# Performance work log

Measured on AMD Instinct MI355X. Metric: run time of the kernel, lower is better.

## Reference

```python
import jax, jax.numpy as jnp
import numpy as np
from jax import lax

S, B, V, D, H, L, C = 2048, 32, 50000, 512, 512, 2, 10


def setup_inputs() -> dict:
    key = jax.random.key(0)
    ks = jax.random.split(key, 6)
    x = jax.random.randint(ks[0], (S, B), 0, V)  # (seq, batch) token ids
    embed = jax.random.normal(ks[1], (V, D), jnp.float32) * 0.1
    # per layer: W maps input -> [x_tilde, f_gate, r_gate], each H wide
    W = jax.random.normal(ks[2], (L, D, 3 * H), jnp.float32) * (1.0 / np.sqrt(D))
    b = jnp.zeros((L, 2 * H), jnp.float32)  # biases for f and r gates
    Wc = jax.random.normal(ks[3], (H, C), jnp.float32) * 0.05
    bc = jnp.zeros((C,), jnp.float32)
    return {"x": x, "embed": embed, "W": W, "b": b, "Wc": Wc, "bc": bc}


def _sru_layer(h_in, W_l, b_l):
    # h_in: (S, B, H) (input dim == hidden dim -> identity highway skip)
    U = jnp.einsum('sbd,dk->sbk', h_in, W_l)  # (S, B, 3H)
    xt, fg, rg = jnp.split(U, 3, axis=-1)
    bf, br = jnp.split(b_l, 2)
    f = jax.nn.sigmoid(fg + bf)
    r = jax.nn.sigmoid(rg + br)

    def step(c, inp):
        f_t, xt_t = inp
        c = f_t * c + (1.0 - f_t) * xt_t  # elementwise light recurrence
        return c, c

    c0 = jnp.zeros((h_in.shape[1], f.shape[-1]), h_in.dtype)
    _, cs = lax.scan(step, c0, (f, xt))  # cs: (S, B, H)
    # highway output
    return r * jnp.tanh(cs) + (1.0 - r) * h_in


def reference(x, embed, W, b, Wc, bc):
    h = embed[x]  # (S, B, D); dropout layers are identity at inference
    for l in range(W.shape[0]):
        h = _sru_layer(h, W[l], b[l])
    out = jnp.tanh(h)            # (S, B, H)
    pooled = jnp.max(out, axis=0)  # max-pool over time -> (B, H)
    pooled = jnp.tanh(pooled)
    return pooled @ Wc + bc      # (B, C)
```

## Files before the change

### kernel.cpp

```cpp
#include <hip/hip_runtime.h>
#include <cmath>

#define S_LEN 2048
#define B_SZ 32
#define D_DIM 512
#define H_DIM 512
#define C_NUM 10
#define M_ROWS (S_LEN * B_SZ)
#define BH (B_SZ * H_DIM)
#define N_COLS (3 * H_DIM)

#define SC 1024
#define SCH 8
#define NSUB 128
#define CROWS (SC * B_SZ)

typedef __bf16 bf16_t;
typedef bf16_t bf16x8 __attribute__((ext_vector_type(8)));
typedef float f32x4 __attribute__((ext_vector_type(4)));
typedef unsigned short ushort_t;

__device__ __forceinline__ unsigned int f2bf(float f) {
  union { float f; unsigned int u; } a;
  a.f = f;
  unsigned int r = a.u + 0x7FFFu + ((a.u >> 16) & 1u);
  return r >> 16;
}
__device__ __forceinline__ unsigned int pack2bf(float lo, float hi) {
  return f2bf(lo) | (f2bf(hi) << 16);
}
__device__ __forceinline__ float bflo(unsigned int u) {
  union { unsigned int u; float f; } a; a.u = u << 16; return a.f;
}
__device__ __forceinline__ float bfhi(unsigned int u) {
  union { unsigned int u; float f; } a; a.u = u & 0xffff0000u; return a.f;
}
__device__ __forceinline__ float sigf(float x) {
  return 1.f / (1.f + __expf(-x));
}
__device__ __forceinline__ float tanh_fast(float c) {
  float e = __expf(2.f * c);
  return 1.f - 2.f / (e + 1.f);
}
__device__ __forceinline__ void load16_lds(const void* g, void* l) {
  __builtin_amdgcn_global_load_lds(
      (const __attribute__((address_space(1))) unsigned int*)g,
      (__attribute__((address_space(3))) unsigned int*)l, 16, 0, 0);
}


__global__ __launch_bounds__(256) void gather_kernel(const int* __restrict__ x,
                                                     const float* __restrict__ embed,
                                                     uint4* __restrict__ E4) {
  int i = blockIdx.x * blockDim.x + threadIdx.x;
  const int total = M_ROWS * 16;
  int stride = gridDim.x * blockDim.x;
  for (; i < total; i += stride) {
    int m = i >> 4;
    int kg = (i & 15) * 4;
    int tile = m >> 7, row = m & 127;
    int xm = x[m];
    const float4* src = (const float4*)(embed + (size_t)xm * 512 + kg * 8);
    float4 v[8];
#pragma unroll
    for (int j = 0; j < 8; j++) v[j] = src[j];
    uint4* dst = E4 + (size_t)tile * 8192 + row;
#pragma unroll
    for (int j = 0; j < 4; j++) {
      dst[(size_t)(kg + j) * 128] =
          make_uint4(pack2bf(v[2 * j].x, v[2 * j].y), pack2bf(v[2 * j].z, v[2 * j].w),
                     pack2bf(v[2 * j + 1].x, v[2 * j + 1].y),
                     pack2bf(v[2 * j + 1].z, v[2 * j + 1].w));
    }
  }
}

__global__ __launch_bounds__(256) void wt_kernel(const float* __restrict__ W,
                                                 ushort_t* __restrict__ Wt) {
  int e = blockIdx.x * blockDim.x + threadIdx.x;
  if (e >= 2 * 786432) return;
  int l = e / 786432;
  int t = e - l * 786432;
  int ntile = t >> 16;
  int rr = t & 65535;
  int kc = rr >> 10;
  int row = (rr >> 3) & 127;
  int kk = t & 7;
  int n = ntile * 128 + row;
  int k = kc * 8 + kk;
  Wt[e] = (ushort_t)f2bf(W[(size_t)l * D_DIM * N_COLS + (size_t)k * N_COLS + n]);
}

__global__ __launch_bounds__(256, 3) void sru_gemm_bf16(
    const ushort_t* __restrict__ At,
    int tile0,
    const ushort_t* __restrict__ Bt,
    ushort_t* __restrict__ xt_out, ushort_t* __restrict__ f_out,
    ushort_t* __restrict__ r_out) {
  __shared__ ushort_t As[3][4096];
  __shared__ ushort_t Bs[3][4096];
  const int t = threadIdx.x;
  const int wave = t >> 6, lane = t & 63;
  const int cpx = gridDim.x >> 3;
  const int swz = (blockIdx.x & 7) * cpx + (blockIdx.x >> 3);
  const int nb = swz % 12, mb = swz / 12;
  const int m0 = mb * 128, n0 = nb * 128;
  const int wm = wave & 1, wn = wave >> 1;
  const int lrow = lane >> 4, lcol = lane & 15;

  f32x4 acc[4][4];
#pragma unroll
  for (int i = 0; i < 4; i++)
#pragma unroll
    for (int j = 0; j < 4; j++) acc[i][j] = (f32x4){0.f, 0.f, 0.f, 0.f};

  const ushort_t* Ab = At + ((size_t)(tile0 + mb) << 16);
  const ushort_t* Bb = Bt + ((size_t)nb << 16);
  const int c0 = wave * 2;
  const int le = lane * 8;

#define STAGE(buf, k0)                                                      \
  do {                                                                      \
    load16_lds(Ab + (k0) * 128 + (c0 + 0) * 512 + le, &As[buf][(c0 + 0) * 512]); \
    load16_lds(Ab + (k0) * 128 + (c0 + 1) * 512 + le, &As[buf][(c0 + 1) * 512]); \
    load16_lds(Bb + (k0) * 128 + (c0 + 0) * 512 + le, &Bs[buf][(c0 + 0) * 512]); \
    load16_lds(Bb + (k0) * 128 + (c0 + 1) * 512 + le, &Bs[buf][(c0 + 1) * 512]); \
  } while (0)

  STAGE(0, 0);
  STAGE(1, 32);
#pragma unroll
  for (int step = 0; step < 16; ++step) {
    if (step < 15)
      asm volatile("s_waitcnt vmcnt(4)" ::: "memory");
    else
      asm volatile("s_waitcnt vmcnt(0)" ::: "memory");
    __builtin_amdgcn_s_barrier();
    asm volatile("" ::: "memory");
    if (step < 14) STAGE((step + 2) % 3, (step + 2) * 32);
    const int cur = step % 3;
    bf16x8 af[4], bfr[4];
#pragma unroll
    for (int mi = 0; mi < 4; mi++)
      af[mi] = *reinterpret_cast<const bf16x8*>(
          &As[cur][(lrow * 128 + wm * 64 + mi * 16 + lcol) * 8]);
#pragma unroll
    for (int ni = 0; ni < 4; ni++)
      bfr[ni] = *reinterpret_cast<const bf16x8*>(
          &Bs[cur][(lrow * 128 + wn * 64 + ni * 16 + lcol) * 8]);
#pragma unroll
    for (int mi = 0; mi < 4; mi++)
#pragma unroll
      for (int ni = 0; ni < 4; ni++)
        acc[mi][ni] = __builtin_amdgcn_mfma_f32_16x16x32_bf16(
            bfr[ni], af[mi], acc[mi][ni], 0, 0, 0);
  }
#undef STAGE

  const int region = n0 >> 9;
  ushort_t* outp = region == 0 ? xt_out : (region == 1 ? f_out : r_out);
  const int nloc0 = (n0 & 511) + wn * 64 + lrow * 4;
#pragma unroll
  for (int mi = 0; mi < 4; mi++) {
    const int m = m0 + wm * 64 + mi * 16 + lcol;
    const size_t mpart = ((size_t)(m >> 7) << 16) + ((size_t)(m & 127) << 3);
#pragma unroll
    for (int ni = 0; ni < 4; ni++) {
      const int nloc = nloc0 + ni * 16;
      size_t ad = mpart + ((size_t)(nloc >> 3) << 10) + (nloc & 7);
      uint2 pk;
      pk.x = pack2bf(acc[mi][ni][0], acc[mi][ni][1]);
      pk.y = pack2bf(acc[mi][ni][2], acc[mi][ni][3]);
      *(uint2*)&outp[ad] = pk;
    }
  }
}

template <int LAST>
__global__ __launch_bounds__(1024) void scan_fused(
    const ushort_t* __restrict__ f, const ushort_t* __restrict__ xt,
    const ushort_t* __restrict__ r, const ushort_t* __restrict__ hw,
    ushort_t* __restrict__ ob, const float* __restrict__ bl,
    float* __restrict__ cstate, float* __restrict__ pmax,
    int first, int m0abs) {
  __shared__ float sA[8][NSUB][8];
  __shared__ float sB[8][NSUB][8];
  const int tid = threadIdx.x;
  const int q = tid & 7, ch = tid >> 3;
  const int p = blockIdx.x * 8 + q;
  const int hc = p >> 5, b = p & 31;
  const int h0 = hc << 3;
  float bf_[8];
#pragma unroll
  for (int j = 0; j < 8; j++) bf_[j] = bl[h0 + j];

  {
    float Aa[8], Bv[8];
#pragma unroll
    for (int j = 0; j < 8; j++) { Aa[j] = 1.f; Bv[j] = 0.f; }
    for (int s = 0; s < SCH; s++) {
      int ml = ((ch * SCH + s) << 5) + b;
      size_t ga = ((size_t)(ml >> 7) << 16) + ((size_t)hc << 10) + ((ml & 127) << 3);
      uint4 fq = *(const uint4*)&f[ga];
      uint4 xq = *(const uint4*)&xt[ga];
      unsigned int fw[4] = {fq.x, fq.y, fq.z, fq.w};
      unsigned int xw[4] = {xq.x, xq.y, xq.z, xq.w};
#pragma unroll
      for (int w = 0; w < 4; w++) {
        float fa = sigf(bflo(fw[w]) + bf_[2 * w]);
        float fb = sigf(bfhi(fw[w]) + bf_[2 * w + 1]);
        Bv[2 * w]     = fa * Bv[2 * w]     + (1.f - fa) * bflo(xw[w]);
        Bv[2 * w + 1] = fb * Bv[2 * w + 1] + (1.f - fb) * bfhi(xw[w]);
        Aa[2 * w] *= fa;
        Aa[2 * w + 1] *= fb;
      }
    }
#pragma unroll
    for (int j = 0; j < 8; j++) { sA[j][ch][q] = Aa[j]; sB[j][ch][q] = Bv[j]; }
  }
  __syncthreads();

  if (tid < 64) {
    int qq = tid & 7, jj = tid >> 3;
    int pp = blockIdx.x * 8 + qq;
    int bb = pp & 31, hh = (pp >> 5) * 8 + jj;
    float c = first ? 0.f : cstate[bb * 512 + hh];
    for (int cc = 0; cc < NSUB; cc++) {
      float a = sA[jj][cc][qq];
      float bv = sB[jj][cc][qq];
      sA[jj][cc][qq] = c;
      c = a * c + bv;
    }
    cstate[bb * 512 + hh] = c;
  }
  __syncthreads();

  float br_[8];
#pragma unroll
  for (int j = 0; j < 8; j++) br_[j] = bl[512 + h0 + j];
  float c[8], pm[8];
#pragma unroll
  for (int j = 0; j < 8; j++) { c[j] = sA[j][ch][q]; pm[j] = -1e30f; }
  for (int s = 0; s < SCH; s++) {
    int ml = ((ch * SCH + s) << 5) + b;
    size_t ga = ((size_t)(ml >> 7) << 16) + ((size_t)hc << 10) + ((ml & 127) << 3);
    int ma = m0abs + ml;
    size_t ha = ((size_t)(ma >> 7) << 16) + ((size_t)hc << 10) + ((ma & 127) << 3);
    uint4 fq = *(const uint4*)&f[ga];
    uint4 xq = *(const uint4*)&xt[ga];
    uint4 rq = *(const uint4*)&r[ga];
    uint4 hq = *(const uint4*)&hw[ha];
    unsigned int fw[4] = {fq.x, fq.y, fq.z, fq.w};
    unsigned int xw[4] = {xq.x, xq.y, xq.z, xq.w};
    unsigned int rw[4] = {rq.x, rq.y, rq.z, rq.w};
    unsigned int hv[4] = {hq.x, hq.y, hq.z, hq.w};
    unsigned int ow[4];
#pragma unroll
    for (int w = 0; w < 4; w++) {
      float fa = sigf(bflo(fw[w]) + bf_[2 * w]);
      float fb = sigf(bfhi(fw[w]) + bf_[2 * w + 1]);
      float ra = sigf(bflo(rw[w]) + br_[2 * w]);
      float rb = sigf(bfhi(rw[w]) + br_[2 * w + 1]);
      c[2 * w]     = fa * c[2 * w]     + (1.f - fa) * bflo(xw[w]);
      c[2 * w + 1] = fb * c[2 * w + 1] + (1.f - fb) * bfhi(xw[w]);
      float oa = ra * tanh_fast(c[2 * w]) + (1.f - ra) * bflo(hv[w]);
      float obv = rb * tanh_fast(c[2 * w + 1]) + (1.f - rb) * bfhi(hv[w]);
      if (LAST) {
        pm[2 * w] = fmaxf(pm[2 * w], oa);
        pm[2 * w + 1] = fmaxf(pm[2 * w + 1], obv);
      } else {
        ow[w] = pack2bf(oa, obv);
      }
    }
    if (!LAST) *(uint4*)&ob[ha] = make_uint4(ow[0], ow[1], ow[2], ow[3]);
  }
  if (LAST) {
    int lin = ch * BH + b * 512 + h0;
    if (first) {
#pragma unroll
      for (int j = 0; j < 8; j++) pmax[lin + j] = pm[j];
    } else {
#pragma unroll
      for (int j = 0; j < 8; j++) pmax[lin + j] = fmaxf(pmax[lin + j], pm[j]);
    }
  }
}

__global__ void pool_kernel(const float* __restrict__ pmax, float* __restrict__ pooled) {
  int rem = blockIdx.x * blockDim.x + threadIdx.x;
  float m = -1e30f;
  for (int ch = 0; ch < NSUB; ch++) m = fmaxf(m, pmax[ch * BH + rem]);
  pooled[rem] = tanhf(tanhf(m));
}

__global__ void out_gemm(const float* __restrict__ pooled, const float* __restrict__ Wc,
                         const float* __restrict__ bc, float* __restrict__ out) {
  __shared__ float pt[H_DIM];
  int b = blockIdx.x;
  for (int i = threadIdx.x; i < H_DIM; i += blockDim.x) pt[i] = pooled[b * H_DIM + i];
  __syncthreads();
  if (threadIdx.x < C_NUM) {
    int c = threadIdx.x;
    float acc = bc[c];
    for (int hh = 0; hh < H_DIM; hh++) acc = fmaf(pt[hh], Wc[hh * C_NUM + c], acc);
    out[b * C_NUM + c] = acc;
  }
}

extern "C" void kernel_launch(void* const* d_in, const int* in_sizes, int n_in,
                              void* d_out, int out_size, void* d_ws, size_t ws_size,
                              hipStream_t stream) {
  const int* x = (const int*)d_in[0];
  const float* embed = (const float*)d_in[1];
  const float* W = (const float*)d_in[2];
  const float* b = (const float*)d_in[3];
  const float* Wc = (const float*)d_in[4];
  const float* bc = (const float*)d_in[5];
  float* out = (float*)d_out;

  const size_t SZ_HB = (size_t)M_ROWS * H_DIM * 2;
  const size_t SZ_G  = (size_t)CROWS * H_DIM * 2;
  const size_t SZ_WT = 2ull * N_COLS * D_DIM * 2;
  const size_t SZ_BHf = (size_t)BH * 4;

  char* p = (char*)d_ws;
  float* cstate0 = (float*)p; p += SZ_BHf;
  float* cstate1 = (float*)p; p += SZ_BHf;
  float* pooled  = (float*)p; p += SZ_BHf;
  float* pmax    = (float*)p; p += (size_t)NSUB * SZ_BHf;
  ushort_t* Wt   = (ushort_t*)p; p += SZ_WT;
  ushort_t* E    = (ushort_t*)p; p += SZ_HB;
  ushort_t* OB   = (ushort_t*)p; p += SZ_HB;
  ushort_t* X0   = (ushort_t*)p; p += SZ_G;
  ushort_t* F0   = (ushort_t*)p; p += SZ_G;
  ushort_t* R0   = (ushort_t*)p;

  gather_kernel<<<4096, 256, 0, stream>>>(x, embed, (uint4*)E);
  wt_kernel<<<6144, 256, 0, stream>>>(W, Wt);

  const int gemm_blocks = (CROWS / 128) * (N_COLS / 128);
  const int NOUTER = S_LEN / SC;
  const float* bl0 = b;
  const float* bl1 = b + 2 * H_DIM;
  const ushort_t* Wt0 = Wt;
  const ushort_t* Wt1 = Wt + (size_t)N_COLS * D_DIM;

  for (int ci = 0; ci < NOUTER; ci++) {
    const int m0abs = ci * CROWS;
    const int tile0 = m0abs >> 7;
    sru_gemm_bf16<<<gemm_blocks, 256, 0, stream>>>(E, tile0, Wt0, X0, F0, R0);
    scan_fused<0><<<256, 1024, 0, stream>>>(F0, X0, R0, E, OB, bl0, cstate0,
                                            nullptr, ci == 0, m0abs);
    sru_gemm_bf16<<<gemm_blocks, 256, 0, stream>>>(OB, tile0, Wt1, X0, F0, R0);
    scan_fused<1><<<256, 1024, 0, stream>>>(F0, X0, R0, OB, nullptr, bl1, cstate1,
                                            pmax, ci == 0, m0abs);
  }

  pool_kernel<<<BH / 256, 256, 0, stream>>>(pmax, pooled);
  out_gemm<<<B_SZ, 256, 0, stream>>>(pooled, Wc, bc, out);
}
```

Baseline: 537.9 us.

## Switch GEMM to double-buffered 64-deep K tiles with syncthreads pipeline

The bf16 GEMM moves from a triple-buffered 32-wide K pipeline with manual vmcnt waits to a double-buffered pipeline with 64-wide K chunks. This halves the number of barriers per tile and issues larger loads per stage. The cost is more LDS per block (64KB), which lowers occupancy from 3 to 2 blocks per CU. __syncthreads also waits on every outstanding load, so prefetch overlap may shrink.

After: 542.5 us. No clear change (+0.9%).

```diff
diff --git a/kernel.cpp b/kernel.cpp
--- a/kernel.cpp
+++ b/kernel.cpp
@@ -91,14 +91,14 @@
   Wt[e] = (ushort_t)f2bf(W[(size_t)l * D_DIM * N_COLS + (size_t)k * N_COLS + n]);
 }
 
-__global__ __launch_bounds__(256, 3) void sru_gemm_bf16(
+__global__ __launch_bounds__(256, 2) void sru_gemm_bf16(
     const ushort_t* __restrict__ At,
     int tile0,
     const ushort_t* __restrict__ Bt,
     ushort_t* __restrict__ xt_out, ushort_t* __restrict__ f_out,
     ushort_t* __restrict__ r_out) {
-  __shared__ ushort_t As[3][4096];
-  __shared__ ushort_t Bs[3][4096];
+  __shared__ ushort_t As[2][8192];
+  __shared__ ushort_t Bs[2][8192];
   const int t = threadIdx.x;
   const int wave = t >> 6, lane = t & 63;
   const int cpx = gridDim.x >> 3;
@@ -116,44 +116,45 @@
 
   const ushort_t* Ab = At + ((size_t)(tile0 + mb) << 16);
   const ushort_t* Bb = Bt + ((size_t)nb << 16);
-  const int c0 = wave * 2;
   const int le = lane * 8;
 
-#define STAGE(buf, k0)                                                      \
-  do {                                                                      \
-    load16_lds(Ab + (k0) * 128 + (c0 + 0) * 512 + le, &As[buf][(c0 + 0) * 512]); \
-    load16_lds(Ab + (k0) * 128 + (c0 + 1) * 512 + le, &As[buf][(c0 + 1) * 512]); \
-    load16_lds(Bb + (k0) * 128 + (c0 + 0) * 512 + le, &Bs[buf][(c0 + 0) * 512]); \
-    load16_lds(Bb + (k0) * 128 + (c0 + 1) * 512 + le, &Bs[buf][(c0 + 1) * 512]); \
+#define STAGE(buf, k0)                                                    \
+  do {                                                                    \
+    _Pragma("unroll")                                                     \
+    for (int rr = 0; rr < 4; ++rr) {                                      \
+      const int cb = (rr * 4 + wave) * 512;                               \
+      load16_lds(Ab + (size_t)(k0) * 128 + cb + le, &As[buf][cb]);        \
+      load16_lds(Bb + (size_t)(k0) * 128 + cb + le, &Bs[buf][cb]);        \
+    }                                                                     \
   } while (0)
 
   STAGE(0, 0);
-  STAGE(1, 32);
-#pragma unroll
-  for (int step = 0; step < 16; ++step) {
-    if (step < 15)
-      asm volatile("s_waitcnt vmcnt(4)" ::: "memory");
-    else
-      asm volatile("s_waitcnt vmcnt(0)" ::: "memory");
-    __builtin_amdgcn_s_barrier();
-    asm volatile("" ::: "memory");
-    if (step < 14) STAGE((step + 2) % 3, (step + 2) * 32);
-    const int cur = step % 3;
-    bf16x8 af[4], bfr[4];
-#pragma unroll
-    for (int mi = 0; mi < 4; mi++)
-      af[mi] = *reinterpret_cast<const bf16x8*>(
-          &As[cur][(lrow * 128 + wm * 64 + mi * 16 + lcol) * 8]);
-#pragma unroll
-    for (int ni = 0; ni < 4; ni++)
-      bfr[ni] = *reinterpret_cast<const bf16x8*>(
-          &Bs[cur][(lrow * 128 + wn * 64 + ni * 16 + lcol) * 8]);
-#pragma unroll
-    for (int mi = 0; mi < 4; mi++)
+  __syncthreads();
+#pragma unroll
+  for (int step = 0; step < 8; ++step) {
+    if (step < 7) STAGE((step + 1) & 1, (step + 1) * 64);
+    const int cur = step & 1;
+    bf16x8 af[2][4], bfr[2][4];
+#pragma unroll
+    for (int ks = 0; ks < 2; ks++) {
+#pragma unroll
+      for (int mi = 0; mi < 4; mi++)
+        af[ks][mi] = *reinterpret_cast<const bf16x8*>(
+            &As[cur][((ks * 4 + lrow) * 128 + wm * 64 + mi * 16 + lcol) * 8]);
 #pragma unroll
       for (int ni = 0; ni < 4; ni++)
-        acc[mi][ni] = __builtin_amdgcn_mfma_f32_16x16x32_bf16(
-            bfr[ni], af[mi], acc[mi][ni], 0, 0, 0);
+        bfr[ks][ni] = *reinterpret_cast<const bf16x8*>(
+            &Bs[cur][((ks * 4 + lrow) * 128 + wn * 64 + ni * 16 + lcol) * 8]);
+    }
+#pragma unroll
+    for (int ks = 0; ks < 2; ks++)
+#pragma unroll
+      for (int mi = 0; mi < 4; mi++)
+#pragma unroll
+        for (int ni = 0; ni < 4; ni++)
+          acc[mi][ni] = __builtin_amdgcn_mfma_f32_16x16x32_bf16(
+              bfr[ks][ni], af[ks][mi], acc[mi][ni], 0, 0, 0);
+    __syncthreads();
   }
 #undef STAGE
 
```

## Enlarge GEMM tile to 256x128 with 8 waves and 64-wide K stages

Applied to the files above, without the earlier changes.

Rewrites the bf16 GEMM to use 512-thread blocks computing 256x128 output tiles, halving the number of blocks, and stages K in 64-element chunks with a triple-buffered LDS pipeline (8 iterations instead of 16). The bigger M tile shares each B tile across twice as many rows and the deeper stages mean fewer barriers per FLOP. In exchange it uses much more LDS per block (about 144KB), which limits occupancy, and it relies on the waitcnt counts matching the extra loads per stage.

Measured after the change: 540.4 us. About the same (+0.5%).

```diff
diff --git a/kernel.cpp b/kernel.cpp
--- a/kernel.cpp
+++ b/kernel.cpp
@@ -91,21 +91,21 @@
   Wt[e] = (ushort_t)f2bf(W[(size_t)l * D_DIM * N_COLS + (size_t)k * N_COLS + n]);
 }
 
-__global__ __launch_bounds__(256, 3) void sru_gemm_bf16(
+__global__ __launch_bounds__(512, 2) void sru_gemm_bf16(
     const ushort_t* __restrict__ At,
     int tile0,
     const ushort_t* __restrict__ Bt,
     ushort_t* __restrict__ xt_out, ushort_t* __restrict__ f_out,
     ushort_t* __restrict__ r_out) {
-  __shared__ ushort_t As[3][4096];
-  __shared__ ushort_t Bs[3][4096];
+  __shared__ ushort_t As[3][16384];
+  __shared__ ushort_t Bs[3][8192];
   const int t = threadIdx.x;
   const int wave = t >> 6, lane = t & 63;
   const int cpx = gridDim.x >> 3;
   const int swz = (blockIdx.x & 7) * cpx + (blockIdx.x >> 3);
   const int nb = swz % 12, mb = swz / 12;
-  const int m0 = mb * 128, n0 = nb * 128;
-  const int wm = wave & 1, wn = wave >> 1;
+  const int m0 = mb * 256, n0 = nb * 128;
+  const int wm = wave >> 1, wn = wave & 1;
   const int lrow = lane >> 4, lcol = lane & 15;
 
   f32x4 acc[4][4];
@@ -114,46 +114,65 @@
 #pragma unroll
     for (int j = 0; j < 4; j++) acc[i][j] = (f32x4){0.f, 0.f, 0.f, 0.f};
 
-  const ushort_t* Ab = At + ((size_t)(tile0 + mb) << 16);
+  const ushort_t* Ab = At + ((size_t)(tile0 + mb * 2) << 16);
   const ushort_t* Bb = Bt + ((size_t)nb << 16);
-  const int c0 = wave * 2;
+  const int wv = wave * 512;
   const int le = lane * 8;
 
-#define STAGE(buf, k0)                                                      \
-  do {                                                                      \
-    load16_lds(Ab + (k0) * 128 + (c0 + 0) * 512 + le, &As[buf][(c0 + 0) * 512]); \
-    load16_lds(Ab + (k0) * 128 + (c0 + 1) * 512 + le, &As[buf][(c0 + 1) * 512]); \
-    load16_lds(Bb + (k0) * 128 + (c0 + 0) * 512 + le, &Bs[buf][(c0 + 0) * 512]); \
-    load16_lds(Bb + (k0) * 128 + (c0 + 1) * 512 + le, &Bs[buf][(c0 + 1) * 512]); \
+#define STAGE(s, kt)                                                          \
+  do {                                                                        \
+    load16_lds(Ab + (size_t)(kt) * 8192 + 0 * 4096 + wv + le,                 \
+               &As[s][0 * 8192 + 0 * 4096 + wv]);                             \
+    load16_lds(Ab + (size_t)(kt) * 8192 + 1 * 4096 + wv + le,                 \
+               &As[s][0 * 8192 + 1 * 4096 + wv]);                             \
+    load16_lds(Ab + 65536 + (size_t)(kt) * 8192 + 0 * 4096 + wv + le,         \
+               &As[s][1 * 8192 + 0 * 4096 + wv]);                             \
+    load16_lds(Ab + 65536 + (size_t)(kt) * 8192 + 1 * 4096 + wv + le,         \
+               &As[s][1 * 8192 + 1 * 4096 + wv]);                             \
+    load16_lds(Bb + (size_t)(kt) * 8192 + 0 * 4096 + wv + le,                 \
+               &Bs[s][0 * 4096 + wv]);                                        \
+    load16_lds(Bb + (size_t)(kt) * 8192 + 1 * 4096 + wv + le,                 \
+               &Bs[s][1 * 4096 + wv]);                                        \
   } while (0)
 
+  const int a_mt = wm >> 1;
+  const int a_row0 = (wm & 1) * 64;
   STAGE(0, 0);
-  STAGE(1, 32);
-#pragma unroll
-  for (int step = 0; step < 16; ++step) {
-    if (step < 15)
-      asm volatile("s_waitcnt vmcnt(4)" ::: "memory");
+  STAGE(1, 1);
+
+#pragma unroll
+  for (int kt = 0; kt < 8; ++kt) {
+    const int s = kt % 3;
+    __builtin_amdgcn_s_barrier();
+    asm volatile("" ::: "memory");
+    if (kt < 6) STAGE((kt + 2) % 3, kt + 2);
+    if (kt < 6)
+      asm volatile("s_waitcnt vmcnt(12)" ::: "memory");
+    else if (kt == 6)
+      asm volatile("s_waitcnt vmcnt(6)" ::: "memory");
     else
       asm volatile("s_waitcnt vmcnt(0)" ::: "memory");
     __builtin_amdgcn_s_barrier();
     asm volatile("" ::: "memory");
-    if (step < 14) STAGE((step + 2) % 3, (step + 2) * 32);
-    const int cur = step % 3;
-    bf16x8 af[4], bfr[4];
-#pragma unroll
-    for (int mi = 0; mi < 4; mi++)
-      af[mi] = *reinterpret_cast<const bf16x8*>(
-          &As[cur][(lrow * 128 + wm * 64 + mi * 16 + lcol) * 8]);
-#pragma unroll
-    for (int ni = 0; ni < 4; ni++)
-      bfr[ni] = *reinterpret_cast<const bf16x8*>(
-          &Bs[cur][(lrow * 128 + wn * 64 + ni * 16 + lcol) * 8]);
-#pragma unroll
-    for (int mi = 0; mi < 4; mi++)
+#pragma unroll
+    for (int ks = 0; ks < 2; ++ks) {
+      const int kc = ks * 4 + lrow;
+      bf16x8 af[4], bfr[4];
+#pragma unroll
+      for (int mi = 0; mi < 4; mi++)
+        af[mi] = *reinterpret_cast<const bf16x8*>(
+            &As[s][a_mt * 8192 + kc * 1024 + (a_row0 + mi * 16 + lcol) * 8]);
 #pragma unroll
       for (int ni = 0; ni < 4; ni++)
-        acc[mi][ni] = __builtin_amdgcn_mfma_f32_16x16x32_bf16(
-            bfr[ni], af[mi], acc[mi][ni], 0, 0, 0);
+        bfr[ni] = *reinterpret_cast<const bf16x8*>(
+            &Bs[s][kc * 1024 + (wn * 64 + ni * 16 + lcol) * 8]);
+#pragma unroll
+      for (int mi = 0; mi < 4; mi++)
+#pragma unroll
+        for (int ni = 0; ni < 4; ni++)
+          acc[mi][ni] = __builtin_amdgcn_mfma_f32_16x16x32_bf16(
+              bfr[ni], af[mi], acc[mi][ni], 0, 0, 0);
+    }
   }
 #undef STAGE
 
@@ -338,7 +357,7 @@
   gather_kernel<<<4096, 256, 0, stream>>>(x, embed, (uint4*)E);
   wt_kernel<<<6144, 256, 0, stream>>>(W, Wt);
 
-  const int gemm_blocks = (CROWS / 128) * (N_COLS / 128);
+  const int gemm_blocks = (CROWS / 256) * (N_COLS / 128);
   const int NOUTER = S_LEN / SC;
   const float* bl0 = b;
   const float* bl1 = b + 2 * H_DIM;
@@ -348,10 +367,10 @@
   for (int ci = 0; ci < NOUTER; ci++) {
     const int m0abs = ci * CROWS;
     const int tile0 = m0abs >> 7;
-    sru_gemm_bf16<<<gemm_blocks, 256, 0, stream>>>(E, tile0, Wt0, X0, F0, R0);
+    sru_gemm_bf16<<<gemm_blocks, 512, 0, stream>>>(E, tile0, Wt0, X0, F0, R0);
     scan_fused<0><<<256, 1024, 0, stream>>>(F0, X0, R0, E, OB, bl0, cstate0,
                                             nullptr, ci == 0, m0abs);
-    sru_gemm_bf16<<<gemm_blocks, 256, 0, stream>>>(OB, tile0, Wt1, X0, F0, R0);
+    sru_gemm_bf16<<<gemm_blocks, 512, 0, stream>>>(OB, tile0, Wt1, X0, F0, R0);
     scan_fused<1><<<256, 1024, 0, stream>>>(F0, X0, R0, OB, nullptr, bl1, cstate1,
                                             pmax, ci == 0, m0abs);
   }
```

## Make GEMM blocks loop over four M tiles with double-buffered LDS

Applied to the files above, without the earlier changes.

Each GEMM block now handles four consecutive 128-row M tiles in one persistent loop, so the grid is a quarter of its former size. The block writes out and resets its accumulators after each tile. Staging drops from a triple-buffered vmcnt pipeline to a double buffer with __syncthreads each step, which cuts LDS use. The aim is to amortize block launch and prologue cost and reuse B-tile locality. The risk is less parallelism (768 blocks), weaker latency hiding from the simpler pipeline, and extra barriers.

Result: slower. 581.5 us (+8.1%).

```diff
diff --git a/kernel.cpp b/kernel.cpp
--- a/kernel.cpp
+++ b/kernel.cpp
@@ -97,14 +97,14 @@
     const ushort_t* __restrict__ Bt,
     ushort_t* __restrict__ xt_out, ushort_t* __restrict__ f_out,
     ushort_t* __restrict__ r_out) {
-  __shared__ ushort_t As[3][4096];
-  __shared__ ushort_t Bs[3][4096];
+  __shared__ ushort_t As[2][4096];
+  __shared__ ushort_t Bs[2][4096];
   const int t = threadIdx.x;
   const int wave = t >> 6, lane = t & 63;
   const int cpx = gridDim.x >> 3;
   const int swz = (blockIdx.x & 7) * cpx + (blockIdx.x >> 3);
-  const int nb = swz % 12, mb = swz / 12;
-  const int m0 = mb * 128, n0 = nb * 128;
+  const int nb = swz % 12, mg = swz / 12;
+  const int n0 = nb * 128;
   const int wm = wave & 1, wn = wave >> 1;
   const int lrow = lane >> 4, lcol = lane & 15;
 
@@ -114,31 +114,31 @@
 #pragma unroll
     for (int j = 0; j < 4; j++) acc[i][j] = (f32x4){0.f, 0.f, 0.f, 0.f};
 
-  const ushort_t* Ab = At + ((size_t)(tile0 + mb) << 16);
+  const ushort_t* Abase = At + ((size_t)(tile0 + mg * 4) << 16);
   const ushort_t* Bb = Bt + ((size_t)nb << 16);
   const int c0 = wave * 2;
   const int le = lane * 8;
 
-#define STAGE(buf, k0)                                                      \
-  do {                                                                      \
-    load16_lds(Ab + (k0) * 128 + (c0 + 0) * 512 + le, &As[buf][(c0 + 0) * 512]); \
-    load16_lds(Ab + (k0) * 128 + (c0 + 1) * 512 + le, &As[buf][(c0 + 1) * 512]); \
-    load16_lds(Bb + (k0) * 128 + (c0 + 0) * 512 + le, &Bs[buf][(c0 + 0) * 512]); \
-    load16_lds(Bb + (k0) * 128 + (c0 + 1) * 512 + le, &Bs[buf][(c0 + 1) * 512]); \
+  const int region = n0 >> 9;
+  ushort_t* outp = region == 0 ? xt_out : (region == 1 ? f_out : r_out);
+  const int nloc0 = (n0 & 511) + wn * 64 + lrow * 4;
+
+#define STAGE(buf, g)                                                         \
+  do {                                                                        \
+    const size_t aoff = ((size_t)((g) >> 4) << 16) + (size_t)((g) & 15) * 4096; \
+    const size_t boff = (size_t)((g) & 15) * 4096;                            \
+    load16_lds(Abase + aoff + (c0 + 0) * 512 + le, &As[buf][(c0 + 0) * 512]); \
+    load16_lds(Abase + aoff + (c0 + 1) * 512 + le, &As[buf][(c0 + 1) * 512]); \
+    load16_lds(Bb + boff + (c0 + 0) * 512 + le, &Bs[buf][(c0 + 0) * 512]);    \
+    load16_lds(Bb + boff + (c0 + 1) * 512 + le, &Bs[buf][(c0 + 1) * 512]);    \
   } while (0)
 
   STAGE(0, 0);
-  STAGE(1, 32);
-#pragma unroll
-  for (int step = 0; step < 16; ++step) {
-    if (step < 15)
-      asm volatile("s_waitcnt vmcnt(4)" ::: "memory");
-    else
-      asm volatile("s_waitcnt vmcnt(0)" ::: "memory");
-    __builtin_amdgcn_s_barrier();
-    asm volatile("" ::: "memory");
-    if (step < 14) STAGE((step + 2) % 3, (step + 2) * 32);
-    const int cur = step % 3;
+  __syncthreads();
+#pragma unroll 16
+  for (int step = 0; step < 64; ++step) {
+    if (step + 1 < 64) STAGE((step + 1) & 1, step + 1);
+    const int cur = step & 1;
     bf16x8 af[4], bfr[4];
 #pragma unroll
     for (int mi = 0; mi < 4; mi++)
@@ -154,26 +154,27 @@
       for (int ni = 0; ni < 4; ni++)
         acc[mi][ni] = __builtin_amdgcn_mfma_f32_16x16x32_bf16(
             bfr[ni], af[mi], acc[mi][ni], 0, 0, 0);
+    __syncthreads();
+    if ((step & 15) == 15) {
+      const int mtile = mg * 4 + (step >> 4);
+#pragma unroll
+      for (int mi = 0; mi < 4; mi++) {
+        const int m = mtile * 128 + wm * 64 + mi * 16 + lcol;
+        const size_t mpart = ((size_t)(m >> 7) << 16) + ((size_t)(m & 127) << 3);
+#pragma unroll
+        for (int ni = 0; ni < 4; ni++) {
+          const int nloc = nloc0 + ni * 16;
+          size_t ad = mpart + ((size_t)(nloc >> 3) << 10) + (nloc & 7);
+          uint2 pk;
+          pk.x = pack2bf(acc[mi][ni][0], acc[mi][ni][1]);
+          pk.y = pack2bf(acc[mi][ni][2], acc[mi][ni][3]);
+          *(uint2*)&outp[ad] = pk;
+          acc[mi][ni] = (f32x4){0.f, 0.f, 0.f, 0.f};
+        }
+      }
+    }
   }
 #undef STAGE
-
-  const int region = n0 >> 9;
-  ushort_t* outp = region == 0 ? xt_out : (region == 1 ? f_out : r_out);
-  const int nloc0 = (n0 & 511) + wn * 64 + lrow * 4;
-#pragma unroll
-  for (int mi = 0; mi < 4; mi++) {
-    const int m = m0 + wm * 64 + mi * 16 + lcol;
-    const size_t mpart = ((size_t)(m >> 7) << 16) + ((size_t)(m & 127) << 3);
-#pragma unroll
-    for (int ni = 0; ni < 4; ni++) {
-      const int nloc = nloc0 + ni * 16;
-      size_t ad = mpart + ((size_t)(nloc >> 3) << 10) + (nloc & 7);
-      uint2 pk;
-      pk.x = pack2bf(acc[mi][ni][0], acc[mi][ni][1]);
-      pk.y = pack2bf(acc[mi][ni][2], acc[mi][ni][3]);
-      *(uint2*)&outp[ad] = pk;
-    }
-  }
 }
 
 template <int LAST>
@@ -338,7 +339,7 @@
   gather_kernel<<<4096, 256, 0, stream>>>(x, embed, (uint4*)E);
   wt_kernel<<<6144, 256, 0, stream>>>(W, Wt);
 
-  const int gemm_blocks = (CROWS / 128) * (N_COLS / 128);
+  const int gemm_blocks = (CROWS / 512) * (N_COLS / 128);
   const int NOUTER = S_LEN / SC;
   const float* bl0 = b;
   const float* bl1 = b + 2 * H_DIM;
```
